# Kernel optimization log

Hardware: AMD Instinct MI355X
Metric: run time of the kernel (lower is better)

The kernel has to match this reference:

```python
import jax, jax.numpy as jnp
import numpy as np

D_MODEL = 1024
N_HEADS = 16
HEAD_DIM = D_MODEL // N_HEADS


def setup_inputs() -> dict:
    key = jax.random.key(0)
    ks = jax.random.split(key, 5)
    B, T = 2, 2048
    x = jax.random.normal(ks[0], (B, T, D_MODEL), dtype=jnp.float32)
    s = 1.0 / np.sqrt(D_MODEL)
    qkv_w = jax.random.uniform(ks[1], (3 * D_MODEL, D_MODEL), jnp.float32, -s, s)
    qkv_b = jax.random.uniform(ks[2], (3 * D_MODEL,), jnp.float32, -s, s)
    out_w = jax.random.uniform(ks[3], (D_MODEL, D_MODEL), jnp.float32, -s, s)
    out_b = jax.random.uniform(ks[4], (D_MODEL,), jnp.float32, -s, s)
    return {"x": x, "qkv_w": qkv_w, "qkv_b": qkv_b, "out_w": out_w, "out_b": out_b}


def reference(x, qkv_w, qkv_b, out_w, out_b):
    B, T, _ = x.shape
    # qkv projection: [B,T,3*D]
    qkv = x @ qkv_w.T + qkv_b
    qkv = qkv.reshape(B, T, 3, N_HEADS, HEAD_DIM)
    qkv = jnp.transpose(qkv, (2, 0, 3, 1, 4))  # [3,B,H,T,Hd]
    q, k, v = qkv[0], qkv[1], qkv[2]
    scale = 1.0 / np.sqrt(HEAD_DIM)
    scores = jnp.einsum("bhqd,bhkd->bhqk", q, k) * scale  # [B,H,T,T]
    causal = jnp.tril(jnp.ones((T, T), dtype=bool))
    scores = jnp.where(causal, scores, -jnp.inf)
    weights = jax.nn.softmax(scores, axis=-1)
    # dropout in eval mode (identity)
    out = jnp.einsum("bhqk,bhkd->bhqd", weights, v)  # [B,H,T,Hd]
    out = jnp.transpose(out, (0, 2, 1, 3)).reshape(B, T, D_MODEL)
    return out @ out_w.T + out_b
```

## Files before the change

### kernel.cpp

```cpp
#include <hip/hip_runtime.h>
#include <hip/hip_bf16.h>


typedef __bf16 bf16;
typedef bf16 bf16x8 __attribute__((ext_vector_type(8)));
typedef bf16 bf16x4 __attribute__((ext_vector_type(4)));
typedef float f32x4 __attribute__((ext_vector_type(4)));

#define MFMA16(a, b, c) __builtin_amdgcn_mfma_f32_16x16x32_bf16((a), (b), (c), 0, 0, 0)

static constexpr int D_MODEL = 1024;
static constexpr int NH = 16;
static constexpr int HD = 64;
static constexpr int SEQ = 2048;
static constexpr int NB = 2;
static constexpr float QSCALE = 0.125f * 1.44269504088896340736f;

__device__ __forceinline__ bf16x8 cvt8(const float* p) {
    float4 u0 = *(const float4*)p;
    float4 u1 = *(const float4*)(p + 4);
    bf16x8 v = { (bf16)u0.x, (bf16)u0.y, (bf16)u0.z, (bf16)u0.w,
                 (bf16)u1.x, (bf16)u1.y, (bf16)u1.z, (bf16)u1.w };
    return v;
}

__device__ __forceinline__ void async16(const bf16* g, bf16* l) {
    __builtin_amdgcn_global_load_lds(
        (const __attribute__((address_space(1))) void*)g,
        (__attribute__((address_space(3))) void*)l, 16, 0, 0);
}

__global__ __launch_bounds__(256)
void k_cast(const float* __restrict__ in, bf16* __restrict__ out, int n8)
{
    int i = blockIdx.x * 256 + threadIdx.x;
    if (i < n8) *(bf16x8*)&out[(size_t)i * 8] = cvt8(&in[(size_t)i * 8]);
}

__global__ __launch_bounds__(256)
void k_qkv(const bf16* __restrict__ x, const bf16* __restrict__ w,
           const float* __restrict__ bias,
           bf16* __restrict__ Qb, bf16* __restrict__ Kb, bf16* __restrict__ VbT)
{
    __shared__ bf16 As[128 * 32];
    __shared__ bf16 Ws[128 * 32];

    const int tid  = threadIdx.x;
    const int wv   = tid >> 6;
    const int lane = tid & 63;
    const int lr   = lane & 15;
    const int lk   = lane >> 4;
    const int wm   = wv >> 1, wn = wv & 1;
    const int m0   = blockIdx.x * 128;
    const int n0   = blockIdx.y * 128;

    const int sRow = tid >> 2;
    const int sCol = (tid & 3) * 8;
    const int sOff = sRow * 32 + sCol;

    f32x4 acc[4][4] = {};

    for (int kt = 0; kt < 1024; kt += 32) {
        __syncthreads();
        async16(&x[(size_t)(m0 + sRow     ) * 1024 + kt + sCol], &As[sOff]);
        async16(&x[(size_t)(m0 + 64 + sRow) * 1024 + kt + sCol], &As[64 * 32 + sOff]);
        async16(&w[(size_t)(n0 + sRow     ) * 1024 + kt + sCol], &Ws[sOff]);
        async16(&w[(size_t)(n0 + 64 + sRow) * 1024 + kt + sCol], &Ws[64 * 32 + sOff]);
        __syncthreads();

        bf16x8 a[4], b[4];
        #pragma unroll
        for (int i = 0; i < 4; i++) {
            a[i] = *(const bf16x8*)&As[(wm * 64 + i * 16 + lr) * 32 + lk * 8];
            b[i] = *(const bf16x8*)&Ws[(wn * 64 + i * 16 + lr) * 32 + lk * 8];
        }
        #pragma unroll
        for (int i = 0; i < 4; i++)
            #pragma unroll
            for (int j = 0; j < 4; j++)
                acc[i][j] = MFMA16(a[i], b[j], acc[i][j]);
    }

    #pragma unroll
    for (int i = 0; i < 4; i++) {
        #pragma unroll
        for (int j = 0; j < 4; j++) {
            const int gm0 = m0 + wm * 64 + i * 16 + lk * 4;
            const int gn  = n0 + wn * 64 + j * 16 + lr;
            const int sel = gn >> 10;
            const int rem = gn & 1023;
            const int h   = rem >> 6;
            const int hd  = rem & 63;
            const int bb  = gm0 >> 11;
            const int t0  = gm0 & 2047;
            if (sel == 2) {
                bf16x4 p;
                #pragma unroll
                for (int r = 0; r < 4; r++) p[r] = (bf16)(acc[i][j][r] + bias[gn]);
                *(bf16x4*)&VbT[((size_t)(bb * NH + h) * HD + hd) * SEQ + t0] = p;
            } else {
                #pragma unroll
                for (int r = 0; r < 4; r++) {
                    float v = acc[i][j][r] + bias[gn];
                    size_t idx = ((size_t)(bb * NH + h) * SEQ + t0 + r) * HD + hd;
                    if (sel == 0) Qb[idx] = (bf16)(v * QSCALE);
                    else          Kb[idx] = (bf16)v;
                }
            }
        }
    }
}

__global__ __launch_bounds__(128, 2)
void k_attn(const bf16* __restrict__ Qb, const bf16* __restrict__ Kb,
            const bf16* __restrict__ VbT, bf16* __restrict__ AO)
{
    __shared__ bf16 Ps[64][72];

    const int tid  = threadIdx.x;
    const int wv   = tid >> 6;
    const int lane = tid & 63;
    const int lr   = lane & 15;
    const int lk   = lane >> 4;

    const int id = blockIdx.x;
    const int c_ = id & 255;
    const int bh = c_ & 31;
    const int u  = c_ >> 5;
    const int k2 = id >> 8;
    const int qt = (k2 & 1) ? (k2 * 8 + 7 - u) : (k2 * 8 + u);

    const bf16* Qp  = Qb  + (size_t)bh * SEQ * HD;
    const bf16* Kp  = Kb  + (size_t)bh * SEQ * HD;
    const bf16* Vtp = VbT + (size_t)bh * HD * SEQ;

    const int qbase = qt * 64 + wv * 32;
    const int qg[2] = { qbase + lr, qbase + 16 + lr };

    bf16x8 qf[2][2];
    #pragma unroll
    for (int h = 0; h < 2; h++)
        #pragma unroll
        for (int c = 0; c < 2; c++)
            qf[h][c] = *(const bf16x8*)&Qp[(size_t)(qbase + h * 16 + lr) * HD + c * 32 + lk * 8];

    f32x4 ot[2][4] = {};
    float lsum[2] = { 0.f, 0.f };

    bf16x8 ka[4][2], kn[4][2], va[4][2];

    #pragma unroll
    for (int j = 0; j < 4; j++)
        #pragma unroll
        for (int c = 0; c < 2; c++)
            ka[j][c] = *(const bf16x8*)&Kp[(size_t)(j * 16 + lr) * HD + c * 32 + lk * 8];

    auto body = [&](int kt, bf16x8 (&kc)[4][2], bf16x8 (&knx)[4][2]) {
        const int k0 = kt * 64;

        #pragma unroll
        for (int jh = 0; jh < 4; jh++)
            #pragma unroll
            for (int c = 0; c < 2; c++)
                va[jh][c] = *(const bf16x8*)&Vtp[(size_t)(jh * 16 + lr) * SEQ + k0 + c * 32 + lk * 8];

        if (kt < qt) {
            #pragma unroll
            for (int j = 0; j < 4; j++)
                #pragma unroll
                for (int c = 0; c < 2; c++)
                    knx[j][c] = *(const bf16x8*)&Kp[(size_t)(k0 + 64 + j * 16 + lr) * HD + c * 32 + lk * 8];
        }

        f32x4 s[2][4] = {};
        #pragma unroll
        for (int j = 0; j < 4; j++) {
            #pragma unroll
            for (int c = 0; c < 2; c++) {
                s[0][j] = MFMA16(kc[j][c], qf[0][c], s[0][j]);
                s[1][j] = MFMA16(kc[j][c], qf[1][c], s[1][j]);
            }
        }

        #pragma unroll
        for (int h = 0; h < 2; h++) {
            float rs[4];
            #pragma unroll
            for (int j = 0; j < 4; j++) {
                const int keyb = k0 + j * 16 + lk * 4;
                f32x4 p;
                #pragma unroll
                for (int r = 0; r < 4; r++) {
                    float e = __builtin_amdgcn_exp2f(s[h][j][r]);
                    if (kt == qt) e = (keyb + r > qg[h]) ? 0.f : e;
                    p[r] = e;
                }
                s[h][j] = p;
                rs[j] = (p[0] + p[1]) + (p[2] + p[3]);
            }
            lsum[h] += (rs[0] + rs[1]) + (rs[2] + rs[3]);
        }

        #pragma unroll
        for (int h = 0; h < 2; h++)
            #pragma unroll
            for (int j = 0; j < 4; j++) {
                bf16x4 p4 = { (bf16)s[h][j][0], (bf16)s[h][j][1],
                              (bf16)s[h][j][2], (bf16)s[h][j][3] };
                *(bf16x4*)&Ps[wv * 32 + h * 16 + lr][j * 16 + lk * 4] = p4;
            }

        #pragma unroll
        for (int c = 0; c < 2; c++) {
            bf16x8 pb0 = *(const bf16x8*)&Ps[wv * 32      + lr][c * 32 + lk * 8];
            bf16x8 pb1 = *(const bf16x8*)&Ps[wv * 32 + 16 + lr][c * 32 + lk * 8];
            #pragma unroll
            for (int jh = 0; jh < 4; jh++) {
                ot[0][jh] = MFMA16(va[jh][c], pb0, ot[0][jh]);
                ot[1][jh] = MFMA16(va[jh][c], pb1, ot[1][jh]);
            }
        }
    };

    int kt = 0;
    for (;;) {
        body(kt, ka, kn);
        if (kt == qt) break;
        kt++;
        body(kt, kn, ka);
        if (kt == qt) break;
        kt++;
    }

    #pragma unroll
    for (int h = 0; h < 2; h++) {
        lsum[h] += __shfl_xor(lsum[h], 16);
        lsum[h] += __shfl_xor(lsum[h], 32);
    }

    const int b_ = bh >> 4, h_ = bh & 15;
    #pragma unroll
    for (int h = 0; h < 2; h++) {
        const float inv = 1.0f / lsum[h];
        const int q = qbase + h * 16 + lr;
        const size_t base = ((size_t)(b_ * SEQ + q)) * D_MODEL + h_ * HD;
        #pragma unroll
        for (int jh = 0; jh < 4; jh++) {
            bf16x4 o4 = { (bf16)(ot[h][jh][0] * inv), (bf16)(ot[h][jh][1] * inv),
                          (bf16)(ot[h][jh][2] * inv), (bf16)(ot[h][jh][3] * inv) };
            *(bf16x4*)&AO[base + jh * 16 + lk * 4] = o4;
        }
    }
}

__global__ __launch_bounds__(256)
void k_oproj(const bf16* __restrict__ a_, const bf16* __restrict__ w,
             const float* __restrict__ bias, float* __restrict__ out)
{
    __shared__ bf16 As[128 * 32];
    __shared__ bf16 Ws[64 * 32];

    const int tid  = threadIdx.x;
    const int wv   = tid >> 6;
    const int lane = tid & 63;
    const int lr   = lane & 15;
    const int lk   = lane >> 4;
    const int wm   = wv >> 1, wn = wv & 1;
    const int m0   = blockIdx.x * 128;
    const int n0   = blockIdx.y * 64;

    const int sRow = tid >> 2;
    const int sCol = (tid & 3) * 8;
    const int sOff = sRow * 32 + sCol;

    f32x4 acc[4][2] = {};

    for (int kt = 0; kt < 1024; kt += 32) {
        __syncthreads();
        async16(&a_[(size_t)(m0 + sRow     ) * 1024 + kt + sCol], &As[sOff]);
        async16(&a_[(size_t)(m0 + 64 + sRow) * 1024 + kt + sCol], &As[64 * 32 + sOff]);
        async16(&w [(size_t)(n0 + sRow     ) * 1024 + kt + sCol], &Ws[sOff]);
        __syncthreads();

        bf16x8 a[4], b[2];
        #pragma unroll
        for (int i = 0; i < 4; i++)
            a[i] = *(const bf16x8*)&As[(wm * 64 + i * 16 + lr) * 32 + lk * 8];
        #pragma unroll
        for (int j = 0; j < 2; j++)
            b[j] = *(const bf16x8*)&Ws[(wn * 32 + j * 16 + lr) * 32 + lk * 8];
        #pragma unroll
        for (int i = 0; i < 4; i++)
            #pragma unroll
            for (int j = 0; j < 2; j++)
                acc[i][j] = MFMA16(a[i], b[j], acc[i][j]);
    }

    #pragma unroll
    for (int i = 0; i < 4; i++) {
        #pragma unroll
        for (int j = 0; j < 2; j++) {
            #pragma unroll
            for (int r = 0; r < 4; r++) {
                int gm = m0 + wm * 64 + i * 16 + lk * 4 + r;
                int gn = n0 + wn * 32 + j * 16 + lr;
                out[(size_t)gm * 1024 + gn] = acc[i][j][r] + bias[gn];
            }
        }
    }
}

extern "C" void kernel_launch(void* const* d_in, const int* in_sizes, int n_in,
                              void* d_out, int out_size, void* d_ws, size_t ws_size,
                              hipStream_t stream)
{
    const float* x     = (const float*)d_in[0];
    const float* qkv_w = (const float*)d_in[1];
    const float* qkv_b = (const float*)d_in[2];
    const float* out_w = (const float*)d_in[3];
    const float* out_b = (const float*)d_in[4];
    float* out = (float*)d_out;

    const size_t SZ = (size_t)NB * NH * SEQ * HD;
    bf16* Qb  = (bf16*)d_ws;
    bf16* Kb  = Qb + SZ;
    bf16* VbT = Kb + SZ;
    bf16* AO  = VbT + SZ;
    bf16* xb  = AO + SZ;
    bf16* wqb = xb + SZ;
    bf16* wob = wqb + (size_t)3 * D_MODEL * D_MODEL;

    hipLaunchKernelGGL(k_cast, dim3(2048), dim3(256), 0, stream, x,     xb,  524288);
    hipLaunchKernelGGL(k_cast, dim3(1536), dim3(256), 0, stream, qkv_w, wqb, 393216);
    hipLaunchKernelGGL(k_cast, dim3(512),  dim3(256), 0, stream, out_w, wob, 131072);

    hipLaunchKernelGGL(k_qkv, dim3(32, 24), dim3(256), 0, stream,
                       xb, wqb, qkv_b, Qb, Kb, VbT);
    hipLaunchKernelGGL(k_attn, dim3(1024), dim3(128), 0, stream,
                       Qb, Kb, VbT, AO);
    hipLaunchKernelGGL(k_oproj, dim3(32, 16), dim3(256), 0, stream,
                       AO, wob, out_b, out);
}
```

Baseline: 205.9 us.

## Split attention key loop across four waves per 32-query tile with LDS reduction

Result: slower. 273.8 us (+33.0%).

```diff
diff --git a/kernel.cpp b/kernel.cpp
--- a/kernel.cpp
+++ b/kernel.cpp
@@ -111,11 +111,13 @@
     }
 }
 
-__global__ __launch_bounds__(128, 2)
+__global__ __launch_bounds__(256, 3)
 void k_attn(const bf16* __restrict__ Qb, const bf16* __restrict__ Kb,
             const bf16* __restrict__ VbT, bf16* __restrict__ AO)
 {
-    __shared__ bf16 Ps[64][72];
+    __shared__ bf16  Ps[128][72];
+    __shared__ float cb[64][33];
+    __shared__ float lsb[32];
 
     const int tid  = threadIdx.x;
     const int wv   = tid >> 6;
@@ -123,18 +125,20 @@
     const int lr   = lane & 15;
     const int lk   = lane >> 4;
 
-    const int id = blockIdx.x;
-    const int c_ = id & 255;
-    const int bh = c_ & 31;
-    const int u  = c_ >> 5;
-    const int k2 = id >> 8;
-    const int qt = (k2 & 1) ? (k2 * 8 + 7 - u) : (k2 * 8 + u);
+    const int id  = blockIdx.x;
+    const int bh  = id & 31;
+    const int qq  = 63 - (id >> 5);
+    const int nkt = (qq >> 1) + 1;
+
+    for (int i = tid; i < 64 * 33; i += 256) (&cb[0][0])[i] = 0.f;
+    if (tid < 32) lsb[tid] = 0.f;
+    __syncthreads();
 
     const bf16* Qp  = Qb  + (size_t)bh * SEQ * HD;
     const bf16* Kp  = Kb  + (size_t)bh * SEQ * HD;
     const bf16* Vtp = VbT + (size_t)bh * HD * SEQ;
 
-    const int qbase = qt * 64 + wv * 32;
+    const int qbase = qq * 32;
     const int qg[2] = { qbase + lr, qbase + 16 + lr };
 
     bf16x8 qf[2][2];
@@ -147,40 +151,29 @@
     f32x4 ot[2][4] = {};
     float lsum[2] = { 0.f, 0.f };
 
-    bf16x8 ka[4][2], kn[4][2], va[4][2];
-
-    #pragma unroll
-    for (int j = 0; j < 4; j++)
-        #pragma unroll
-        for (int c = 0; c < 2; c++)
-            ka[j][c] = *(const bf16x8*)&Kp[(size_t)(j * 16 + lr) * HD + c * 32 + lk * 8];
-
-    auto body = [&](int kt, bf16x8 (&kc)[4][2], bf16x8 (&knx)[4][2]) {
+    for (int kt = wv; kt < nkt; kt += 4) {
         const int k0 = kt * 64;
 
-        #pragma unroll
-        for (int jh = 0; jh < 4; jh++)
-            #pragma unroll
-            for (int c = 0; c < 2; c++)
-                va[jh][c] = *(const bf16x8*)&Vtp[(size_t)(jh * 16 + lr) * SEQ + k0 + c * 32 + lk * 8];
-
-        if (kt < qt) {
-            #pragma unroll
-            for (int j = 0; j < 4; j++)
-                #pragma unroll
-                for (int c = 0; c < 2; c++)
-                    knx[j][c] = *(const bf16x8*)&Kp[(size_t)(k0 + 64 + j * 16 + lr) * HD + c * 32 + lk * 8];
-        }
+        bf16x8 ka[4][2], va[4][2];
+        #pragma unroll
+        for (int j = 0; j < 4; j++)
+            #pragma unroll
+            for (int c = 0; c < 2; c++) {
+                ka[j][c] = *(const bf16x8*)&Kp[(size_t)(k0 + j * 16 + lr) * HD + c * 32 + lk * 8];
+                va[j][c] = *(const bf16x8*)&Vtp[(size_t)(j * 16 + lr) * SEQ + k0 + c * 32 + lk * 8];
+            }
 
         f32x4 s[2][4] = {};
         #pragma unroll
         for (int j = 0; j < 4; j++) {
             #pragma unroll
             for (int c = 0; c < 2; c++) {
-                s[0][j] = MFMA16(kc[j][c], qf[0][c], s[0][j]);
-                s[1][j] = MFMA16(kc[j][c], qf[1][c], s[1][j]);
-            }
-        }
+                s[0][j] = MFMA16(ka[j][c], qf[0][c], s[0][j]);
+                s[1][j] = MFMA16(ka[j][c], qf[1][c], s[1][j]);
+            }
+        }
+
+        const bool diag = (kt == nkt - 1);
 
         #pragma unroll
         for (int h = 0; h < 2; h++) {
@@ -192,7 +185,7 @@
                 #pragma unroll
                 for (int r = 0; r < 4; r++) {
                     float e = __builtin_amdgcn_exp2f(s[h][j][r]);
-                    if (kt == qt) e = (keyb + r > qg[h]) ? 0.f : e;
+                    if (diag) e = (keyb + r > qg[h]) ? 0.f : e;
                     p[r] = e;
                 }
                 s[h][j] = p;
@@ -220,36 +213,31 @@
                 ot[1][jh] = MFMA16(va[jh][c], pb1, ot[1][jh]);
             }
         }
-    };
-
-    int kt = 0;
-    for (;;) {
-        body(kt, ka, kn);
-        if (kt == qt) break;
-        kt++;
-        body(kt, kn, ka);
-        if (kt == qt) break;
-        kt++;
     }
 
     #pragma unroll
     for (int h = 0; h < 2; h++) {
         lsum[h] += __shfl_xor(lsum[h], 16);
         lsum[h] += __shfl_xor(lsum[h], 32);
-    }
-
-    const int b_ = bh >> 4, h_ = bh & 15;
-    #pragma unroll
-    for (int h = 0; h < 2; h++) {
-        const float inv = 1.0f / lsum[h];
-        const int q = qbase + h * 16 + lr;
-        const size_t base = ((size_t)(b_ * SEQ + q)) * D_MODEL + h_ * HD;
-        #pragma unroll
-        for (int jh = 0; jh < 4; jh++) {
-            bf16x4 o4 = { (bf16)(ot[h][jh][0] * inv), (bf16)(ot[h][jh][1] * inv),
-                          (bf16)(ot[h][jh][2] * inv), (bf16)(ot[h][jh][3] * inv) };
-            *(bf16x4*)&AO[base + jh * 16 + lk * 4] = o4;
-        }
+        if (lk == 0) atomicAdd(&lsb[h * 16 + lr], lsum[h]);
+        #pragma unroll
+        for (int jh = 0; jh < 4; jh++)
+            #pragma unroll
+            for (int r = 0; r < 4; r++)
+                atomicAdd(&cb[jh * 16 + lk * 4 + r][h * 16 + lr], ot[h][jh][r]);
+    }
+    __syncthreads();
+
+    {
+        const int b_ = bh >> 4, h_ = bh & 15;
+        const int ql = tid >> 3;
+        const int hc = (tid & 7) * 8;
+        const float inv = 1.0f / lsb[ql];
+        bf16x8 o8;
+        #pragma unroll
+        for (int e = 0; e < 8; e++) o8[e] = (bf16)(cb[hc + e][ql] * inv);
+        const size_t base = ((size_t)(b_ * SEQ + qbase + ql)) * D_MODEL + h_ * HD + hc;
+        *(bf16x8*)&AO[base] = o8;
     }
 }
 
@@ -336,7 +324,7 @@
 
     hipLaunchKernelGGL(k_qkv, dim3(32, 24), dim3(256), 0, stream,
                        xb, wqb, qkv_b, Qb, Kb, VbT);
-    hipLaunchKernelGGL(k_attn, dim3(1024), dim3(128), 0, stream,
+    hipLaunchKernelGGL(k_attn, dim3(2048), dim3(256), 0, stream,
                        Qb, Kb, VbT, AO);
     hipLaunchKernelGGL(k_oproj, dim3(32, 16), dim3(256), 0, stream,
                        AO, wob, out_b, out);
```
